# Kernel tuning notes

Hardware: AMD Instinct MI355X
Metric: run time of the kernel (lower is better)

The kernel has to match this reference:

```python
import jax, jax.numpy as jnp
import numpy as np

D_TOKEN = 256
HIDDEN = max(D_TOKEN // 4, 16)  # 64


def setup_inputs() -> dict:
    key = jax.random.key(0)
    k0, k1, k2, k3, k4, k5, k6 = jax.random.split(key, 7)
    B, N, D, H = 256, 1024, D_TOKEN, HIDDEN
    feature_tokens = jax.random.normal(k0, (B, N, D), dtype=jnp.float32)
    ln_gamma = jnp.ones((D,), dtype=jnp.float32)
    ln_beta = jnp.zeros((D,), dtype=jnp.float32)
    W1 = jax.random.normal(k1, (D, H), dtype=jnp.float32) * (1.0 / np.sqrt(D))
    b1 = jax.random.normal(k2, (H,), dtype=jnp.float32) * 0.01
    W2 = jax.random.normal(k3, (H,), dtype=jnp.float32) * (1.0 / np.sqrt(H))
    b2 = jax.random.normal(k4, (), dtype=jnp.float32) * 0.01
    return {
        "feature_tokens": feature_tokens,
        "ln_gamma": ln_gamma,
        "ln_beta": ln_beta,
        "W1": W1,
        "b1": b1,
        "W2": W2,
        "b2": b2,
    }


def reference(feature_tokens, ln_gamma, ln_beta, W1, b1, W2, b2):
    # LayerNorm over last dim (eps=1e-5, torch default)
    x = feature_tokens
    mu = jnp.mean(x, axis=-1, keepdims=True)
    var = jnp.mean(jnp.square(x - mu), axis=-1, keepdims=True)
    xn = (x - mu) * jax.lax.rsqrt(var + 1e-5) * ln_gamma + ln_beta
    # small MLP scorer: Linear -> GELU(exact) -> Linear(->1)
    h = jax.nn.gelu(jnp.einsum('bnd,dh->bnh', xn, W1) + b1, approximate=False)
    logits = jnp.einsum('bnh,h->bn', h, W2) + b2  # [B, N]
    weights = jax.nn.softmax(logits, axis=1)
    summary = jnp.einsum('bn,bnd->bd', weights, feature_tokens)
    return summary, weights
```

## Files before the change

### kernel.cpp

```cpp
#include <hip/hip_runtime.h>
#include <math.h>

#define DDIM 256
#define HDIM 64
#define NTOK 1024
#define BDIM 256
#define NCH  16

typedef __attribute__((ext_vector_type(8))) short short8;
typedef __attribute__((ext_vector_type(4))) float f32x4;

__device__ __forceinline__ ushort f2bf(float f) {
    uint u = __float_as_uint(f);
    return (ushort)((u + 0x7FFF + ((u >> 16) & 1)) >> 16);
}
__device__ __forceinline__ float bf2f(ushort b) {
    return __uint_as_float(((uint)b) << 16);
}

__device__ __forceinline__ float erf_fast(float x) {
    float ax = fabsf(x);
    float t  = __builtin_amdgcn_rcpf(fmaf(0.3275911f, ax, 1.0f));
    float e  = __expf(-ax * ax);
    float p  = t * fmaf(t, fmaf(t, fmaf(t, fmaf(t, 1.061405429f, -1.453152027f),
                                        1.421413741f), -0.284496736f), 0.254829592f);
    float r  = fmaf(-p, e, 1.0f);
    return copysignf(r, x);
}

__global__ void k_pre(const float* __restrict__ gamma, const float* __restrict__ beta,
                      const float* __restrict__ W1, const float* __restrict__ b1,
                      float* __restrict__ c12, ushort* __restrict__ ghi,
                      ushort* __restrict__ glo) {
    int tid = threadIdx.x;
    if (blockIdx.x == 0 && tid < HDIM) {
        float s1 = 0.f, s2 = 0.f;
        for (int d = 0; d < DDIM; ++d) {
            float w = W1[d * HDIM + tid];
            s1 = fmaf(gamma[d], w, s1);
            s2 = fmaf(beta[d],  w, s2);
        }
        c12[tid]        = s1;
        c12[HDIM + tid] = s2 + b1[tid];
    }
    int e = blockIdx.x * 256 + tid;
    int j    = e & 7;
    int lane = (e >> 3) & 63;
    int nt   = (e >> 9) & 3;
    int kt   = e >> 11;
    int k = kt * 32 + (lane >> 4) * 8 + j;
    int n = nt * 16 + (lane & 15);
    float g = gamma[k] * W1[k * HDIM + n];
    ushort hi = f2bf(g);
    ushort lo = f2bf(g - bf2f(hi));
    ghi[e] = hi;
    glo[e] = lo;
}

__global__ __launch_bounds__(256) void k_fused(
    const float* __restrict__ x, const float* __restrict__ c12,
    const ushort* __restrict__ ghi, const ushort* __restrict__ glo,
    const float* __restrict__ W2, float* __restrict__ logits,
    float* __restrict__ Sc, float2* __restrict__ ml) {
    __shared__ ushort Xh[64][256];
    __shared__ float  slog[64];
    __shared__ float4 Sw[4][64];
    __shared__ float  lsum[4];

    int tid = threadIdx.x, w = tid >> 6, lane = tid & 63;
    int m = lane & 15, kg = lane >> 4;
    size_t tok0 = (size_t)blockIdx.x * 64;
    size_t wtok = tok0 + (size_t)w * 16;

    const float4* rp  = reinterpret_cast<const float4*>(x + (wtok + m) * DDIM + kg * 8);
    const short8* gph = reinterpret_cast<const short8*>(ghi);
    const short8* gpl = reinterpret_cast<const short8*>(glo);
    char* xh_w = reinterpret_cast<char*>(Xh) + (w * 16 + m) * 512;
    uint  swz  = ((uint)(m & 7)) << 4;

    f32x4 acc[4];
    #pragma unroll
    for (int nt = 0; nt < 4; ++nt) acc[nt] = (f32x4){0.f, 0.f, 0.f, 0.f};

    float s1 = 0.f, s2 = 0.f;

    #pragma unroll
    for (int kt = 0; kt < 8; ++kt) {
        float4 xa = rp[kt * 8];
        float4 xb = rp[kt * 8 + 1];

        s1 += ((xa.x + xa.y) + (xa.z + xa.w)) + ((xb.x + xb.y) + (xb.z + xb.w));
        s2 = fmaf(xa.x, xa.x, s2); s2 = fmaf(xa.y, xa.y, s2);
        s2 = fmaf(xa.z, xa.z, s2); s2 = fmaf(xa.w, xa.w, s2);
        s2 = fmaf(xb.x, xb.x, s2); s2 = fmaf(xb.y, xb.y, s2);
        s2 = fmaf(xb.z, xb.z, s2); s2 = fmaf(xb.w, xb.w, s2);

        uint u0 = __float_as_uint(xa.x), u1 = __float_as_uint(xa.y);
        uint u2 = __float_as_uint(xa.z), u3 = __float_as_uint(xa.w);
        uint u4 = __float_as_uint(xb.x), u5 = __float_as_uint(xb.y);
        uint u6 = __float_as_uint(xb.z), u7 = __float_as_uint(xb.w);

        uint t0 = u0 + 0x7FFFu + ((u0 >> 16) & 1u);
        uint t1 = u1 + 0x7FFFu + ((u1 >> 16) & 1u);
        uint t2 = u2 + 0x7FFFu + ((u2 >> 16) & 1u);
        uint t3 = u3 + 0x7FFFu + ((u3 >> 16) & 1u);
        uint t4 = u4 + 0x7FFFu + ((u4 >> 16) & 1u);
        uint t5 = u5 + 0x7FFFu + ((u5 >> 16) & 1u);
        uint t6 = u6 + 0x7FFFu + ((u6 >> 16) & 1u);
        uint t7 = u7 + 0x7FFFu + ((u7 >> 16) & 1u);

        union { uint4 u; short8 s; } Ah, Al;
        Ah.u.x = (t0 >> 16) | (t1 & 0xFFFF0000u);
        Ah.u.y = (t2 >> 16) | (t3 & 0xFFFF0000u);
        Ah.u.z = (t4 >> 16) | (t5 & 0xFFFF0000u);
        Ah.u.w = (t6 >> 16) | (t7 & 0xFFFF0000u);

        float l0 = xa.x - __uint_as_float(t0 & 0xFFFF0000u);
        float l1 = xa.y - __uint_as_float(t1 & 0xFFFF0000u);
        float l2 = xa.z - __uint_as_float(t2 & 0xFFFF0000u);
        float l3 = xa.w - __uint_as_float(t3 & 0xFFFF0000u);
        float l4 = xb.x - __uint_as_float(t4 & 0xFFFF0000u);
        float l5 = xb.y - __uint_as_float(t5 & 0xFFFF0000u);
        float l6 = xb.z - __uint_as_float(t6 & 0xFFFF0000u);
        float l7 = xb.w - __uint_as_float(t7 & 0xFFFF0000u);
        Al.u.x = (__float_as_uint(l0) >> 16) | (__float_as_uint(l1) & 0xFFFF0000u);
        Al.u.y = (__float_as_uint(l2) >> 16) | (__float_as_uint(l3) & 0xFFFF0000u);
        Al.u.z = (__float_as_uint(l4) >> 16) | (__float_as_uint(l5) & 0xFFFF0000u);
        Al.u.w = (__float_as_uint(l6) >> 16) | (__float_as_uint(l7) & 0xFFFF0000u);

        *reinterpret_cast<uint4*>(xh_w + (((uint)(kt * 64 + kg * 16)) ^ swz)) = Ah.u;

        #pragma unroll
        for (int nt = 0; nt < 4; ++nt) {
            int frag = (kt * 4 + nt) * 64 + lane;
            short8 bh = gph[frag];
            short8 bl = gpl[frag];
            acc[nt] = __builtin_amdgcn_mfma_f32_16x16x32_bf16(Ah.s, bh, acc[nt], 0, 0, 0);
            acc[nt] = __builtin_amdgcn_mfma_f32_16x16x32_bf16(Al.s, bh, acc[nt], 0, 0, 0);
            acc[nt] = __builtin_amdgcn_mfma_f32_16x16x32_bf16(Ah.s, bl, acc[nt], 0, 0, 0);
        }
    }

    s1 += __shfl_xor(s1, 16); s1 += __shfl_xor(s1, 32);
    s2 += __shfl_xor(s2, 16); s2 += __shfl_xor(s2, 32);
    float mu  = s1 * (1.f / DDIM);
    float var = fmaf(-mu, mu, s2 * (1.f / DDIM));
    float sv  = rsqrtf(var + 1e-5f);

    float c1v[4], c2v[4], w2v[4];
    #pragma unroll
    for (int nt = 0; nt < 4; ++nt) {
        c1v[nt] = c12[nt * 16 + m];
        c2v[nt] = c12[HDIM + nt * 16 + m];
        w2v[nt] = W2[nt * 16 + m];
    }
    #pragma unroll
    for (int r = 0; r < 4; ++r) {
        int row = kg * 4 + r;
        float mur = __shfl(mu, row);
        float svr = __shfl(sv, row);
        float v = 0.f;
        #pragma unroll
        for (int nt = 0; nt < 4; ++nt) {
            float pre = fmaf(svr, fmaf(-mur, c1v[nt], acc[nt][r]), c2v[nt]);
            float g   = 0.5f * pre * (1.f + erf_fast(pre * 0.70710678118654752f));
            v = fmaf(g, w2v[nt], v);
        }
        v += __shfl_xor(v, 1); v += __shfl_xor(v, 2);
        v += __shfl_xor(v, 4); v += __shfl_xor(v, 8);
        if (m == 0) {
            slog[w * 16 + row]  = v;
            logits[wtok + row]  = v;
        }
    }
    __syncthreads();

    const float4* sl4 = reinterpret_cast<const float4*>(slog);
    float mc = -1e30f;
    #pragma unroll
    for (int i = 0; i < 16; ++i) {
        float4 q = sl4[i];
        mc = fmaxf(mc, fmaxf(fmaxf(q.x, q.y), fmaxf(q.z, q.w)));
    }

    float4 a4 = {0.f, 0.f, 0.f, 0.f};
    float lw = 0.f;
    const char* xh_r = reinterpret_cast<const char*>(Xh);
    uint cb0 = 8u * (uint)lane;
    #pragma unroll
    for (int r = 0; r < 16; ++r) {
        int row = w * 16 + r;
        float p = __expf(slog[row] - mc);
        lw += p;
        uint2 hb = *reinterpret_cast<const uint2*>(
            xh_r + row * 512 + (cb0 ^ (((uint)(r & 7)) << 4)));
        a4.x = fmaf(p, __uint_as_float(hb.x << 16),         a4.x);
        a4.y = fmaf(p, __uint_as_float(hb.x & 0xFFFF0000u), a4.y);
        a4.z = fmaf(p, __uint_as_float(hb.y << 16),         a4.z);
        a4.w = fmaf(p, __uint_as_float(hb.y & 0xFFFF0000u), a4.w);
    }
    Sw[w][lane] = a4;
    if (lane == 0) lsum[w] = lw;
    __syncthreads();

    if (w == 0) {
        float4 q0 = Sw[0][lane], q1 = Sw[1][lane], q2 = Sw[2][lane], q3 = Sw[3][lane];
        float4 S;
        S.x = (q0.x + q1.x) + (q2.x + q3.x);
        S.y = (q0.y + q1.y) + (q2.y + q3.y);
        S.z = (q0.z + q1.z) + (q2.z + q3.z);
        S.w = (q0.w + q1.w) + (q2.w + q3.w);
        reinterpret_cast<float4*>(Sc + (size_t)blockIdx.x * DDIM)[lane] = S;
        if (lane == 0)
            ml[blockIdx.x] = make_float2(mc, (lsum[0] + lsum[1]) + (lsum[2] + lsum[3]));
    }
}

__global__ __launch_bounds__(256) void k_combine(
    const float* __restrict__ Sc, const float2* __restrict__ ml,
    float* __restrict__ summary, float* __restrict__ wts) {
    int b = blockIdx.x, tid = threadIdx.x;

    float2 mlv[NCH];
    float M = -1e30f;
    #pragma unroll
    for (int c = 0; c < NCH; ++c) { mlv[c] = ml[b * NCH + c]; M = fmaxf(M, mlv[c].x); }
    float ex[NCH];
    float denom = 0.f;
    #pragma unroll
    for (int c = 0; c < NCH; ++c) {
        ex[c] = __expf(mlv[c].x - M);
        denom = fmaf(ex[c], mlv[c].y, denom);
    }
    float inv = 1.f / denom;

    float s = 0.f;
    #pragma unroll
    for (int c = 0; c < NCH; ++c)
        s = fmaf(ex[c], Sc[((size_t)b * NCH + c) * DDIM + tid], s);
    summary[(size_t)b * DDIM + tid] = s * inv;

    float4* wp = reinterpret_cast<float4*>(wts + (size_t)b * NTOK) + tid;
    float4 lg = *wp;
    lg.x = __expf(lg.x - M) * inv;
    lg.y = __expf(lg.y - M) * inv;
    lg.z = __expf(lg.z - M) * inv;
    lg.w = __expf(lg.w - M) * inv;
    *wp = lg;
}

extern "C" void kernel_launch(void* const* d_in, const int* in_sizes, int n_in,
                              void* d_out, int out_size, void* d_ws, size_t ws_size,
                              hipStream_t stream) {
    const float* x     = (const float*)d_in[0];
    const float* gamma = (const float*)d_in[1];
    const float* beta  = (const float*)d_in[2];
    const float* W1    = (const float*)d_in[3];
    const float* b1    = (const float*)d_in[4];
    const float* W2    = (const float*)d_in[5];

    float* out     = (float*)d_out;
    float* summary = out;
    float* wts     = out + (size_t)BDIM * DDIM;

    float*  c12 = (float*)d_ws;
    ushort* ghi = (ushort*)((char*)d_ws + 512);
    ushort* glo = ghi + 16384;
    float*  Sc  = (float*)((char*)d_ws + 512 + 65536);
    float2* ml  = (float2*)((char*)d_ws + 512 + 65536 +
                            (size_t)BDIM * NCH * DDIM * sizeof(float));

    hipLaunchKernelGGL(k_pre, dim3(64), dim3(256), 0, stream,
                       gamma, beta, W1, b1, c12, ghi, glo);
    hipLaunchKernelGGL(k_fused, dim3(BDIM * NTOK / 64), dim3(256), 0, stream,
                       x, c12, ghi, glo, W2, wts, Sc, ml);
    hipLaunchKernelGGL(k_combine, dim3(BDIM), dim3(256), 0, stream,
                       Sc, ml, summary, wts);
}
```

Measured before the change: 90.09 us.

## Stage W1 bf16 fragments through double-buffered LDS shared across waves

```diff
diff --git a/kernel.cpp b/kernel.cpp
--- a/kernel.cpp
+++ b/kernel.cpp
@@ -62,10 +62,13 @@
     const ushort* __restrict__ ghi, const ushort* __restrict__ glo,
     const float* __restrict__ W2, float* __restrict__ logits,
     float* __restrict__ Sc, float2* __restrict__ ml) {
-    __shared__ ushort Xh[64][256];
-    __shared__ float  slog[64];
-    __shared__ float4 Sw[4][64];
-    __shared__ float  lsum[4];
+    __shared__ __align__(16) char smem[49152];
+    ushort (*Xh)[256] = reinterpret_cast<ushort (*)[256]>(smem);
+    short8* GsH  = reinterpret_cast<short8*>(smem + 32768);
+    short8* GsL  = reinterpret_cast<short8*>(smem + 40960);
+    float*  slog = reinterpret_cast<float*>(smem + 32768);
+    float4* Sw   = reinterpret_cast<float4*>(smem + 33280);
+    float*  lsum = reinterpret_cast<float*>(smem + 33280 + 4096);
 
     int tid = threadIdx.x, w = tid >> 6, lane = tid & 63;
     int m = lane & 15, kg = lane >> 4;
@@ -84,8 +87,18 @@
 
     float s1 = 0.f, s2 = 0.f;
 
+    GsH[tid] = gph[tid];
+    GsL[tid] = gpl[tid];
+    __syncthreads();
+
     #pragma unroll
     for (int kt = 0; kt < 8; ++kt) {
+        int cb = (kt & 1) * 256, nb = ((kt & 1) ^ 1) * 256;
+        if (kt < 7) {
+            GsH[nb + tid] = gph[(kt + 1) * 256 + tid];
+            GsL[nb + tid] = gpl[(kt + 1) * 256 + tid];
+        }
+
         float4 xa = rp[kt * 8];
         float4 xb = rp[kt * 8 + 1];
 
@@ -132,13 +145,13 @@
 
         #pragma unroll
         for (int nt = 0; nt < 4; ++nt) {
-            int frag = (kt * 4 + nt) * 64 + lane;
-            short8 bh = gph[frag];
-            short8 bl = gpl[frag];
+            short8 bh = GsH[cb + nt * 64 + lane];
+            short8 bl = GsL[cb + nt * 64 + lane];
             acc[nt] = __builtin_amdgcn_mfma_f32_16x16x32_bf16(Ah.s, bh, acc[nt], 0, 0, 0);
             acc[nt] = __builtin_amdgcn_mfma_f32_16x16x32_bf16(Al.s, bh, acc[nt], 0, 0, 0);
             acc[nt] = __builtin_amdgcn_mfma_f32_16x16x32_bf16(Ah.s, bl, acc[nt], 0, 0, 0);
         }
+        __syncthreads();
     }
 
     s1 += __shfl_xor(s1, 16); s1 += __shfl_xor(s1, 32);
@@ -199,12 +212,13 @@
         a4.z = fmaf(p, __uint_as_float(hb.y << 16),         a4.z);
         a4.w = fmaf(p, __uint_as_float(hb.y & 0xFFFF0000u), a4.w);
     }
-    Sw[w][lane] = a4;
+    Sw[w * 64 + lane] = a4;
     if (lane == 0) lsum[w] = lw;
     __syncthreads();
 
     if (w == 0) {
-        float4 q0 = Sw[0][lane], q1 = Sw[1][lane], q2 = Sw[2][lane], q3 = Sw[3][lane];
+        float4 q0 = Sw[0 * 64 + lane], q1 = Sw[1 * 64 + lane];
+        float4 q2 = Sw[2 * 64 + lane], q3 = Sw[3 * 64 + lane];
         float4 S;
         S.x = (q0.x + q1.x) + (q2.x + q3.x);
         S.y = (q0.y + q1.y) + (q2.y + q3.y);
```

Result: slower. 114.0 us (+26.5%).
